# Performance work log

Hardware: AMD Instinct MI355X
Metric: run time of the kernel (lower is better)

Reference implementation:

```python
import jax, jax.numpy as jnp
from jax import lax
import numpy as np

B, C, H, W = 16, 32, 256, 256
K = 3  # kernel size, padding=1 -> SAME


def setup_inputs() -> dict:
    key = jax.random.key(0)
    k1, k2, k3, k4, k5, k6 = jax.random.split(key, 6)
    x = jax.random.normal(k1, (B, C, H, W), dtype=jnp.float32)
    gate_values = jax.random.uniform(k2, (B, C), dtype=jnp.float32)
    # Stacked per-output-channel Conv2d experts == one [C, C, K, K] conv (OIHW)
    fan_in = C * K * K
    bound = 1.0 / np.sqrt(fan_in)
    w1 = jax.random.uniform(k3, (C, C, K, K), minval=-bound, maxval=bound, dtype=jnp.float32)
    b1 = jax.random.uniform(k4, (C,), minval=-bound, maxval=bound, dtype=jnp.float32)
    w2 = jax.random.uniform(k5, (C, C, K, K), minval=-bound, maxval=bound, dtype=jnp.float32)
    b2 = jax.random.uniform(k6, (C,), minval=-bound, maxval=bound, dtype=jnp.float32)
    return {"x": x, "gate_values": gate_values, "w1": w1, "b1": b1, "w2": w2, "b2": b2}


def _moe_conv(x, w, b, g):
    # x: [B,C,H,W], w: [C,C,K,K] (OIHW), b: [C], g: [B,C] effective gate
    y = lax.conv_general_dilated(
        x, w, window_strides=(1, 1), padding='SAME',
        dimension_numbers=('NCHW', 'OIHW', 'NCHW'))
    y = y + b[None, :, None, None]
    return y * g[:, :, None, None]


def reference(x, gate_values, w1, b1, w2, b2):
    # gate rows with value <= 0 are never written -> output stays zero;
    # selected rows are multiplied by the gate value (bias included).
    g = gate_values * (gate_values > 0).astype(gate_values.dtype)
    h = jax.nn.relu(_moe_conv(x, w1, b1, g))
    h = jax.nn.relu(_moe_conv(h, w2, b2, g))
    return h + x
```

## Files before the change

kernel.cpp:

```cpp
#include <hip/hip_runtime.h>

#define BB 16
#define CC 32
#define HH 256
#define WW 256

#define TW 32
#define TH 8
#define NT 4
#define CIP 36

typedef short bf16x8 __attribute__((ext_vector_type(8)));
typedef float f32x16 __attribute__((ext_vector_type(16)));

struct alignas(8)  U2 { unsigned x, y; };
struct alignas(16) U4 { U2 lo, hi; };

__device__ __forceinline__ unsigned short f2bf(float f) {
    unsigned u = __float_as_uint(f);
    u += 0x7fffu + ((u >> 16) & 1u);
    return (unsigned short)(u >> 16);
}

__device__ __forceinline__ unsigned cvtpk(float lo, float hi) {
    unsigned r;
    asm("v_cvt_pk_bf16_f32 %0, %1, %2" : "=v"(r) : "v"(lo), "v"(hi));
    return r;
}

__global__ void wprep(const float* __restrict__ w1, const float* __restrict__ w2,
                      unsigned short* __restrict__ wq) {
    int idx = blockIdx.x * 256 + threadIdx.x;
    if (idx >= 18 * 2 * 32 * 8) return;
    int j    = idx & 7;
    int n    = (idx >> 3) & 31;
    int half = (idx >> 8) & 1;
    int st   = idx >> 9;
    int s = st & 1, pos = st >> 1;
    int ci = s * 16 + half * 8 + j;
    int src = (n * CC + ci) * 9 + pos;
    wq[idx]        = f2bf(w1[src]);
    wq[9216 + idx] = f2bf(w2[src]);
}

template<bool FIRST>
__device__ __forceinline__ void stage_tile(const void* __restrict__ in, int b, int y0, int x0, int t,
                                           unsigned short (&xs)[TH + 2][TW + 2][CIP])
{
    if (FIRST) {
        const float* xb = (const float*)in + (size_t)b * CC * HH * WW;
        #pragma unroll
        for (int rep = 0; rep < 2; ++rep) {
            int p = rep * 256 + t;
            if (p < (TH + 2) * (TW + 2)) {
                int y  = p / (TW + 2);
                int xx = p - y * (TW + 2);
                int gy = y0 + y - 1, gx = x0 + xx - 1;
                bool inb = (gy >= 0 && gy < HH && gx >= 0 && gx < WW);
                int off = gy * WW + gx;
                #pragma unroll
                for (int c16 = 0; c16 < 2; ++c16) {
                    float v[16];
                    #pragma unroll
                    for (int j = 0; j < 16; ++j) v[j] = 0.f;
                    if (inb) {
                        #pragma unroll
                        for (int j = 0; j < 16; ++j)
                            v[j] = xb[(c16 * 16 + j) * (HH * WW) + off];
                    }
                    #pragma unroll
                    for (int k = 0; k < 4; ++k) {
                        U2 w;
                        w.x = cvtpk(v[4 * k + 0], v[4 * k + 1]);
                        w.y = cvtpk(v[4 * k + 2], v[4 * k + 3]);
                        *(U2*)&xs[y][xx][c16 * 16 + k * 4] = w;
                    }
                }
            }
        }
    } else {
        const unsigned short* hb = (const unsigned short*)in + (size_t)b * HH * WW * CC;
        #pragma unroll
        for (int rep = 0; rep < 6; ++rep) {
            int idx = rep * 256 + t;
            if (idx < (TH + 2) * (TW + 2) * 4) {
                int q = idx & 3;
                int p = idx >> 2;
                int y  = p / (TW + 2);
                int xx = p - y * (TW + 2);
                int gy = y0 + y - 1, gx = x0 + xx - 1;
                U4 v; v.lo = {0u, 0u}; v.hi = {0u, 0u};
                if (gy >= 0 && gy < HH && gx >= 0 && gx < WW)
                    v = *(const U4*)(hb + ((gy * WW + gx) * CC + q * 8));
                *(U2*)&xs[y][xx][q * 8]     = v.lo;
                *(U2*)&xs[y][xx][q * 8 + 4] = v.hi;
            }
        }
    }
}

template<bool FIRST>
__global__ __launch_bounds__(256)
void conv_mfma(const void* __restrict__ in,
               const unsigned short* __restrict__ wq,
               const float* __restrict__ bias,
               const float* __restrict__ gate,
               const float* __restrict__ resid,
               void* __restrict__ out)
{
    __shared__ unsigned short xs[TH + 2][TW + 2][CIP];
    __shared__ float gs[CC], bs[CC];

    const int t     = threadIdx.x;
    const int b     = blockIdx.z;
    const int x0    = blockIdx.x * TW;
    const int ybase = blockIdx.y * (TH * NT);

    if (t < CC) {
        float gv = gate[b * CC + t];
        gs[t] = gv > 0.f ? gv : 0.f;
        bs[t] = bias[t];
    }

    const int lane = t & 63;
    const int wv   = t >> 6;
    const int col  = lane & 31;
    const int half = lane >> 5;
    const int r0 = wv * 2, r1 = wv * 2 + 1;

    bf16x8 wf[18];
    #pragma unroll
    for (int st = 0; st < 18; ++st) {
        U4 w = ((const U4*)wq)[(st * 2 + half) * 32 + col];
        wf[st] = __builtin_bit_cast(bf16x8, w);
    }

    stage_tile<FIRST>(in, b, ybase, x0, t, xs);

    #pragma unroll 1
    for (int s = 0; s < NT; ++s) {
        const int y0 = ybase + s * TH;
        __syncthreads();

        f32x16 acc0 = {0,0,0,0,0,0,0,0,0,0,0,0,0,0,0,0};
        f32x16 acc1 = {0,0,0,0,0,0,0,0,0,0,0,0,0,0,0,0};
        #pragma unroll
        for (int st = 0; st < 18; ++st) {
            const int pos = st >> 1, sb = st & 1;
            const int kh = pos / 3, kw = pos - kh * 3;
            const int ci0 = sb * 16 + half * 8;
            U4 xa, xb;
            xa.lo = *(const U2*)&xs[r0 + kh][col + kw][ci0];
            xa.hi = *(const U2*)&xs[r0 + kh][col + kw][ci0 + 4];
            xb.lo = *(const U2*)&xs[r1 + kh][col + kw][ci0];
            xb.hi = *(const U2*)&xs[r1 + kh][col + kw][ci0 + 4];
            acc0 = __builtin_amdgcn_mfma_f32_32x32x16_bf16(wf[st], __builtin_bit_cast(bf16x8, xa), acc0, 0, 0, 0);
            acc1 = __builtin_amdgcn_mfma_f32_32x32x16_bf16(wf[st], __builtin_bit_cast(bf16x8, xb), acc1, 0, 0, 0);
        }

        __syncthreads();

        if (s + 1 < NT) stage_tile<FIRST>(in, b, y0 + TH, x0, t, xs);

        if (FIRST) {
            unsigned short* ob = (unsigned short*)out + (size_t)b * HH * WW * CC;
            int p0 = ((y0 + r0) * WW + x0 + col) * CC;
            int p1 = ((y0 + r1) * WW + x0 + col) * CC;
            #pragma unroll
            for (int g = 0; g < 4; ++g) {
                int c0 = 8 * g + 4 * half;
                float a0 = fmaxf((acc0[4 * g + 0] + bs[c0 + 0]) * gs[c0 + 0], 0.f);
                float a1 = fmaxf((acc0[4 * g + 1] + bs[c0 + 1]) * gs[c0 + 1], 0.f);
                float a2 = fmaxf((acc0[4 * g + 2] + bs[c0 + 2]) * gs[c0 + 2], 0.f);
                float a3 = fmaxf((acc0[4 * g + 3] + bs[c0 + 3]) * gs[c0 + 3], 0.f);
                U2 w0; w0.x = cvtpk(a0, a1); w0.y = cvtpk(a2, a3);
                *(U2*)(ob + p0 + c0) = w0;
                float c0v = fmaxf((acc1[4 * g + 0] + bs[c0 + 0]) * gs[c0 + 0], 0.f);
                float c1v = fmaxf((acc1[4 * g + 1] + bs[c0 + 1]) * gs[c0 + 1], 0.f);
                float c2v = fmaxf((acc1[4 * g + 2] + bs[c0 + 2]) * gs[c0 + 2], 0.f);
                float c3v = fmaxf((acc1[4 * g + 3] + bs[c0 + 3]) * gs[c0 + 3], 0.f);
                U2 w1; w1.x = cvtpk(c0v, c1v); w1.y = cvtpk(c2v, c3v);
                *(U2*)(ob + p1 + c0) = w1;
            }
        } else {
            float* ob = (float*)out + (size_t)b * CC * HH * WW;
            const float* rb = resid + (size_t)b * CC * HH * WW;
            #pragma unroll
            for (int reg = 0; reg < 16; ++reg) {
                int co = (reg & 3) + 8 * (reg >> 2) + 4 * half;
                int i0 = (co * HH + y0 + r0) * WW + x0 + col;
                int i1 = (co * HH + y0 + r1) * WW + x0 + col;
                float v0 = (acc0[reg] + bs[co]) * gs[co];
                float v1 = (acc1[reg] + bs[co]) * gs[co];
                ob[i0] = fmaxf(v0, 0.f) + rb[i0];
                ob[i1] = fmaxf(v1, 0.f) + rb[i1];
            }
        }
    }
}

extern "C" void kernel_launch(void* const* d_in, const int* in_sizes, int n_in,
                              void* d_out, int out_size, void* d_ws, size_t ws_size,
                              hipStream_t stream) {
    const float* x  = (const float*)d_in[0];
    const float* gv = (const float*)d_in[1];
    const float* w1 = (const float*)d_in[2];
    const float* b1 = (const float*)d_in[3];
    const float* w2 = (const float*)d_in[4];
    const float* b2 = (const float*)d_in[5];
    float* out = (float*)d_out;

    unsigned short* h1 = (unsigned short*)d_ws;
    unsigned short* wq = h1 + (size_t)BB * HH * WW * CC;

    wprep<<<36, 256, 0, stream>>>(w1, w2, wq);

    dim3 grid(WW / TW, HH / (TH * NT), BB);
    conv_mfma<true ><<<grid, 256, 0, stream>>>(x,  wq,        b1, gv, nullptr, h1);
    conv_mfma<false><<<grid, 256, 0, stream>>>(h1, wq + 9216, b2, gv, x,       out);
}
```

Baseline: 336.5 us.

## Fuse both convolutions into one kernel keeping intermediate in shared memory

Replaces the two-kernel pipeline, which wrote and reread a bf16 intermediate tensor in global memory, with a single fused kernel. Each block computes conv1 on an overlapping 34-wide halo tile into a double-buffered shared-memory buffer, then runs conv2 from it, so the intermediate never reaches HBM. The cost is recomputing halo columns (only 30 of 32 output columns are useful per tile, plus overlapping rows between tiles), extra shared memory, doubled weight registers, and more synchronisation per step.

```diff
diff --git a/kernel.cpp b/kernel.cpp
--- a/kernel.cpp
+++ b/kernel.cpp
@@ -5,7 +5,7 @@
 #define HH 256
 #define WW 256
 
-#define TW 32
+#define TWV 30
 #define TH 8
 #define NT 4
 #define CIP 36
@@ -43,159 +43,200 @@
     wq[9216 + idx] = f2bf(w2[src]);
 }
 
-template<bool FIRST>
-__device__ __forceinline__ void stage_tile(const void* __restrict__ in, int b, int y0, int x0, int t,
-                                           unsigned short (&xs)[TH + 2][TW + 2][CIP])
+__global__ __launch_bounds__(256, 2)
+void conv_fused(const float* __restrict__ x,
+                const unsigned short* __restrict__ wq,
+                const float* __restrict__ b1v,
+                const float* __restrict__ b2v,
+                const float* __restrict__ gate,
+                float* __restrict__ out)
 {
-    if (FIRST) {
-        const float* xb = (const float*)in + (size_t)b * CC * HH * WW;
-        #pragma unroll
-        for (int rep = 0; rep < 2; ++rep) {
-            int p = rep * 256 + t;
-            if (p < (TH + 2) * (TW + 2)) {
-                int y  = p / (TW + 2);
-                int xx = p - y * (TW + 2);
-                int gy = y0 + y - 1, gx = x0 + xx - 1;
-                bool inb = (gy >= 0 && gy < HH && gx >= 0 && gx < WW);
-                int off = gy * WW + gx;
-                #pragma unroll
-                for (int c16 = 0; c16 < 2; ++c16) {
-                    float v[16];
-                    #pragma unroll
-                    for (int j = 0; j < 16; ++j) v[j] = 0.f;
-                    if (inb) {
-                        #pragma unroll
-                        for (int j = 0; j < 16; ++j)
-                            v[j] = xb[(c16 * 16 + j) * (HH * WW) + off];
-                    }
-                    #pragma unroll
-                    for (int k = 0; k < 4; ++k) {
-                        U2 w;
-                        w.x = cvtpk(v[4 * k + 0], v[4 * k + 1]);
-                        w.y = cvtpk(v[4 * k + 2], v[4 * k + 3]);
-                        *(U2*)&xs[y][xx][c16 * 16 + k * 4] = w;
-                    }
-                }
-            }
-        }
-    } else {
-        const unsigned short* hb = (const unsigned short*)in + (size_t)b * HH * WW * CC;
-        #pragma unroll
-        for (int rep = 0; rep < 6; ++rep) {
-            int idx = rep * 256 + t;
-            if (idx < (TH + 2) * (TW + 2) * 4) {
-                int q = idx & 3;
-                int p = idx >> 2;
-                int y  = p / (TW + 2);
-                int xx = p - y * (TW + 2);
-                int gy = y0 + y - 1, gx = x0 + xx - 1;
-                U4 v; v.lo = {0u, 0u}; v.hi = {0u, 0u};
-                if (gy >= 0 && gy < HH && gx >= 0 && gx < WW)
-                    v = *(const U4*)(hb + ((gy * WW + gx) * CC + q * 8));
-                *(U2*)&xs[y][xx][q * 8]     = v.lo;
-                *(U2*)&xs[y][xx][q * 8 + 4] = v.hi;
-            }
-        }
-    }
-}
-
-template<bool FIRST>
-__global__ __launch_bounds__(256)
-void conv_mfma(const void* __restrict__ in,
-               const unsigned short* __restrict__ wq,
-               const float* __restrict__ bias,
-               const float* __restrict__ gate,
-               const float* __restrict__ resid,
-               void* __restrict__ out)
-{
-    __shared__ unsigned short xs[TH + 2][TW + 2][CIP];
-    __shared__ float gs[CC], bs[CC];
+    __shared__ unsigned short xs[TH + 2][34][CIP];
+    __shared__ unsigned short hs[2][TH][34][CIP];
+    __shared__ float gs[CC], bs1[CC], bs2[CC];
 
     const int t     = threadIdx.x;
     const int b     = blockIdx.z;
-    const int x0    = blockIdx.x * TW;
+    const int x0    = blockIdx.x * TWV;
     const int ybase = blockIdx.y * (TH * NT);
 
     if (t < CC) {
         float gv = gate[b * CC + t];
-        gs[t] = gv > 0.f ? gv : 0.f;
-        bs[t] = bias[t];
+        gs[t]  = gv > 0.f ? gv : 0.f;
+        bs1[t] = b1v[t];
+        bs2[t] = b2v[t];
     }
 
     const int lane = t & 63;
     const int wv   = t >> 6;
     const int col  = lane & 31;
     const int half = lane >> 5;
-    const int r0 = wv * 2, r1 = wv * 2 + 1;
-
-    bf16x8 wf[18];
+    const int r0 = wv * 2, r1 = r0 + 1;
+
+    bf16x8 wf1[18], wf2[18];
+    const U4* wq1 = (const U4*)wq;
+    const U4* wq2 = (const U4*)(wq + 9216);
     #pragma unroll
     for (int st = 0; st < 18; ++st) {
-        U4 w = ((const U4*)wq)[(st * 2 + half) * 32 + col];
-        wf[st] = __builtin_bit_cast(bf16x8, w);
+        wf1[st] = __builtin_bit_cast(bf16x8, wq1[(st * 2 + half) * 32 + col]);
+        wf2[st] = __builtin_bit_cast(bf16x8, wq2[(st * 2 + half) * 32 + col]);
     }
 
-    stage_tile<FIRST>(in, b, ybase, x0, t, xs);
-
-    #pragma unroll 1
-    for (int s = 0; s < NT; ++s) {
-        const int y0 = ybase + s * TH;
-        __syncthreads();
-
+    const int yA = t / 34,        xA = t - yA * 34;
+    const int pB = 256 + t;
+    const int yB = pB / 34,       xB = pB - yB * 34;
+    const bool hasB = t < 84;
+    const float* xb = x + (size_t)b * CC * HH * WW;
+
+    auto stage = [&](int rowT) {
+        float va[32], vb[32];
+        #pragma unroll
+        for (int j = 0; j < 32; ++j) { va[j] = 0.f; vb[j] = 0.f; }
+        const int gyA = rowT + yA, gxA = x0 - 2 + xA;
+        if (gyA >= 0 && gyA < HH && gxA >= 0 && gxA < WW) {
+            const float* pa = xb + (gyA * WW + gxA);
+            #pragma unroll
+            for (int j = 0; j < 32; ++j) va[j] = pa[j * (HH * WW)];
+        }
+        const int gyB = rowT + yB, gxB = x0 - 2 + xB;
+        if (hasB && gyB >= 0 && gyB < HH && gxB >= 0 && gxB < WW) {
+            const float* pb = xb + (gyB * WW + gxB);
+            #pragma unroll
+            for (int j = 0; j < 32; ++j) vb[j] = pb[j * (HH * WW)];
+        }
+        #pragma unroll
+        for (int k = 0; k < 8; ++k) {
+            U2 w; w.x = cvtpk(va[4 * k + 0], va[4 * k + 1]);
+                  w.y = cvtpk(va[4 * k + 2], va[4 * k + 3]);
+            *(U2*)&xs[yA][xA][4 * k] = w;
+        }
+        if (hasB) {
+            #pragma unroll
+            for (int k = 0; k < 8; ++k) {
+                U2 w; w.x = cvtpk(vb[4 * k + 0], vb[4 * k + 1]);
+                      w.y = cvtpk(vb[4 * k + 2], vb[4 * k + 3]);
+                *(U2*)&xs[yB][xB][4 * k] = w;
+            }
+        }
+    };
+
+    auto conv1_iter = [&](int i) {
         f32x16 acc0 = {0,0,0,0,0,0,0,0,0,0,0,0,0,0,0,0};
         f32x16 acc1 = {0,0,0,0,0,0,0,0,0,0,0,0,0,0,0,0};
+        const unsigned short* xsb0 = &xs[r0][col][half * 8];
+        const unsigned short* xsb1 = &xs[r1][col][half * 8];
         #pragma unroll
         for (int st = 0; st < 18; ++st) {
-            const int pos = st >> 1, sb = st & 1;
+            const int pos = st >> 1, s = st & 1;
             const int kh = pos / 3, kw = pos - kh * 3;
-            const int ci0 = sb * 16 + half * 8;
-            U4 xa, xb;
-            xa.lo = *(const U2*)&xs[r0 + kh][col + kw][ci0];
-            xa.hi = *(const U2*)&xs[r0 + kh][col + kw][ci0 + 4];
-            xb.lo = *(const U2*)&xs[r1 + kh][col + kw][ci0];
-            xb.hi = *(const U2*)&xs[r1 + kh][col + kw][ci0 + 4];
-            acc0 = __builtin_amdgcn_mfma_f32_32x32x16_bf16(wf[st], __builtin_bit_cast(bf16x8, xa), acc0, 0, 0, 0);
-            acc1 = __builtin_amdgcn_mfma_f32_32x32x16_bf16(wf[st], __builtin_bit_cast(bf16x8, xb), acc1, 0, 0, 0);
-        }
-
-        __syncthreads();
-
-        if (s + 1 < NT) stage_tile<FIRST>(in, b, y0 + TH, x0, t, xs);
-
-        if (FIRST) {
-            unsigned short* ob = (unsigned short*)out + (size_t)b * HH * WW * CC;
-            int p0 = ((y0 + r0) * WW + x0 + col) * CC;
-            int p1 = ((y0 + r1) * WW + x0 + col) * CC;
-            #pragma unroll
-            for (int g = 0; g < 4; ++g) {
-                int c0 = 8 * g + 4 * half;
-                float a0 = fmaxf((acc0[4 * g + 0] + bs[c0 + 0]) * gs[c0 + 0], 0.f);
-                float a1 = fmaxf((acc0[4 * g + 1] + bs[c0 + 1]) * gs[c0 + 1], 0.f);
-                float a2 = fmaxf((acc0[4 * g + 2] + bs[c0 + 2]) * gs[c0 + 2], 0.f);
-                float a3 = fmaxf((acc0[4 * g + 3] + bs[c0 + 3]) * gs[c0 + 3], 0.f);
-                U2 w0; w0.x = cvtpk(a0, a1); w0.y = cvtpk(a2, a3);
-                *(U2*)(ob + p0 + c0) = w0;
-                float c0v = fmaxf((acc1[4 * g + 0] + bs[c0 + 0]) * gs[c0 + 0], 0.f);
-                float c1v = fmaxf((acc1[4 * g + 1] + bs[c0 + 1]) * gs[c0 + 1], 0.f);
-                float c2v = fmaxf((acc1[4 * g + 2] + bs[c0 + 2]) * gs[c0 + 2], 0.f);
-                float c3v = fmaxf((acc1[4 * g + 3] + bs[c0 + 3]) * gs[c0 + 3], 0.f);
-                U2 w1; w1.x = cvtpk(c0v, c1v); w1.y = cvtpk(c2v, c3v);
-                *(U2*)(ob + p1 + c0) = w1;
+            const int off = (kh * 34 + kw) * CIP + s * 16;
+            U4 xa, xv;
+            xa.lo = *(const U2*)(xsb0 + off);
+            xa.hi = *(const U2*)(xsb0 + off + 4);
+            xv.lo = *(const U2*)(xsb1 + off);
+            xv.hi = *(const U2*)(xsb1 + off + 4);
+            acc0 = __builtin_amdgcn_mfma_f32_32x32x16_bf16(wf1[st], __builtin_bit_cast(bf16x8, xa), acc0, 0, 0, 0);
+            acc1 = __builtin_amdgcn_mfma_f32_32x32x16_bf16(wf1[st], __builtin_bit_cast(bf16x8, xv), acc1, 0, 0, 0);
+        }
+        const int rowbase = ybase - 1 + 8 * i;
+        const int gR0 = rowbase + r0, gR1 = rowbase + r1;
+        const int gC  = x0 - 1 + col;
+        const bool okC = (unsigned)gC < (unsigned)WW;
+        const bool ok0 = okC && ((unsigned)gR0 < (unsigned)HH);
+        const bool ok1 = okC && ((unsigned)gR1 < (unsigned)HH);
+        unsigned short* h0 = &hs[i & 1][r0][col][0];
+        unsigned short* h1 = &hs[i & 1][r1][col][0];
+        #pragma unroll
+        for (int g = 0; g < 4; ++g) {
+            int c0 = 8 * g + 4 * half;
+            float a0 = fmaxf((acc0[4 * g + 0] + bs1[c0 + 0]) * gs[c0 + 0], 0.f);
+            float a1 = fmaxf((acc0[4 * g + 1] + bs1[c0 + 1]) * gs[c0 + 1], 0.f);
+            float a2 = fmaxf((acc0[4 * g + 2] + bs1[c0 + 2]) * gs[c0 + 2], 0.f);
+            float a3 = fmaxf((acc0[4 * g + 3] + bs1[c0 + 3]) * gs[c0 + 3], 0.f);
+            if (!ok0) { a0 = 0.f; a1 = 0.f; a2 = 0.f; a3 = 0.f; }
+            U2 w0; w0.x = cvtpk(a0, a1); w0.y = cvtpk(a2, a3);
+            *(U2*)(h0 + c0) = w0;
+            float d0 = fmaxf((acc1[4 * g + 0] + bs1[c0 + 0]) * gs[c0 + 0], 0.f);
+            float d1 = fmaxf((acc1[4 * g + 1] + bs1[c0 + 1]) * gs[c0 + 1], 0.f);
+            float d2 = fmaxf((acc1[4 * g + 2] + bs1[c0 + 2]) * gs[c0 + 2], 0.f);
+            float d3 = fmaxf((acc1[4 * g + 3] + bs1[c0 + 3]) * gs[c0 + 3], 0.f);
+            if (!ok1) { d0 = 0.f; d1 = 0.f; d2 = 0.f; d3 = 0.f; }
+            U2 w1; w1.x = cvtpk(d0, d1); w1.y = cvtpk(d2, d3);
+            *(U2*)(h1 + c0) = w1;
+        }
+    };
+
+    auto conv2_iter = [&](int j) {
+        f32x16 acc0 = {0,0,0,0,0,0,0,0,0,0,0,0,0,0,0,0};
+        f32x16 acc1 = {0,0,0,0,0,0,0,0,0,0,0,0,0,0,0,0};
+        const unsigned short* hb0 = &hs[j & 1][0][0][0];
+        const unsigned short* hb1 = &hs[(j + 1) & 1][0][0][0];
+        if (wv < 3) {
+            const unsigned short* p0 = hb0 + (r0 * 34 + col) * CIP + half * 8;
+            const unsigned short* p1 = hb0 + (r1 * 34 + col) * CIP + half * 8;
+            #pragma unroll
+            for (int st = 0; st < 18; ++st) {
+                const int pos = st >> 1, s = st & 1;
+                const int kh = pos / 3, kw = pos - kh * 3;
+                const int off = (kh * 34 + kw) * CIP + s * 16;
+                U4 xa, xv;
+                xa.lo = *(const U2*)(p0 + off);
+                xa.hi = *(const U2*)(p0 + off + 4);
+                xv.lo = *(const U2*)(p1 + off);
+                xv.hi = *(const U2*)(p1 + off + 4);
+                acc0 = __builtin_amdgcn_mfma_f32_32x32x16_bf16(wf2[st], __builtin_bit_cast(bf16x8, xa), acc0, 0, 0, 0);
+                acc1 = __builtin_amdgcn_mfma_f32_32x32x16_bf16(wf2[st], __builtin_bit_cast(bf16x8, xv), acc1, 0, 0, 0);
             }
         } else {
-            float* ob = (float*)out + (size_t)b * CC * HH * WW;
-            const float* rb = resid + (size_t)b * CC * HH * WW;
+            const unsigned short* c0p = hb0 + col * CIP + half * 8;
+            const unsigned short* c1p = hb1 + col * CIP + half * 8;
+            #pragma unroll
+            for (int st = 0; st < 18; ++st) {
+                const int pos = st >> 1, s = st & 1;
+                const int kh = pos / 3, kw = pos - kh * 3;
+                const int q0 = 6 + kh, q1 = 7 + kh;
+                const unsigned short* p0 = (q0 >= 8 ? c1p : c0p) + ((q0 & 7) * 34 + kw) * CIP + s * 16;
+                const unsigned short* p1 = (q1 >= 8 ? c1p : c0p) + ((q1 & 7) * 34 + kw) * CIP + s * 16;
+                U4 xa, xv;
+                xa.lo = *(const U2*)(p0);
+                xa.hi = *(const U2*)(p0 + 4);
+                xv.lo = *(const U2*)(p1);
+                xv.hi = *(const U2*)(p1 + 4);
+                acc0 = __builtin_amdgcn_mfma_f32_32x32x16_bf16(wf2[st], __builtin_bit_cast(bf16x8, xa), acc0, 0, 0, 0);
+                acc1 = __builtin_amdgcn_mfma_f32_32x32x16_bf16(wf2[st], __builtin_bit_cast(bf16x8, xv), acc1, 0, 0, 0);
+            }
+        }
+        const int gO0 = ybase + 8 * j + r0;
+        const int gO1 = gO0 + 1;
+        const int gX  = x0 + col;
+        const bool okN = (col < TWV) && (gX < WW);
+        float* ob = out + (size_t)b * CC * HH * WW;
+        const float* rb = x + (size_t)b * CC * HH * WW;
+        if (okN) {
             #pragma unroll
             for (int reg = 0; reg < 16; ++reg) {
                 int co = (reg & 3) + 8 * (reg >> 2) + 4 * half;
-                int i0 = (co * HH + y0 + r0) * WW + x0 + col;
-                int i1 = (co * HH + y0 + r1) * WW + x0 + col;
-                float v0 = (acc0[reg] + bs[co]) * gs[co];
-                float v1 = (acc1[reg] + bs[co]) * gs[co];
+                int i0 = (co * HH + gO0) * WW + gX;
+                int i1 = (co * HH + gO1) * WW + gX;
+                float v0 = (acc0[reg] + bs2[co]) * gs[co];
+                float v1 = (acc1[reg] + bs2[co]) * gs[co];
                 ob[i0] = fmaxf(v0, 0.f) + rb[i0];
                 ob[i1] = fmaxf(v1, 0.f) + rb[i1];
             }
         }
+    };
+
+    stage(ybase - 2);
+    __syncthreads();
+    conv1_iter(0);
+    #pragma unroll 1
+    for (int i = 1; i <= NT; ++i) {
+        __syncthreads();
+        stage(ybase - 2 + 8 * i);
+        __syncthreads();
+        conv1_iter(i);
+        __syncthreads();
+        conv2_iter(i - 1);
     }
 }
 
@@ -210,12 +251,10 @@
     const float* b2 = (const float*)d_in[5];
     float* out = (float*)d_out;
 
-    unsigned short* h1 = (unsigned short*)d_ws;
-    unsigned short* wq = h1 + (size_t)BB * HH * WW * CC;
+    unsigned short* wq = (unsigned short*)d_ws;
 
     wprep<<<36, 256, 0, stream>>>(w1, w2, wq);
 
-    dim3 grid(WW / TW, HH / (TH * NT), BB);
-    conv_mfma<true ><<<grid, 256, 0, stream>>>(x,  wq,        b1, gv, nullptr, h1);
-    conv_mfma<false><<<grid, 256, 0, stream>>>(h1, wq + 9216, b2, gv, x,       out);
-}
+    dim3 grid((WW + TWV - 1) / TWV, HH / (TH * NT), BB);
+    conv_fused<<<grid, 256, 0, stream>>>(x, wq, b1, b2, gv, out);
+}
```

New measurement: 398.0 us. 18.3% more time.
